# Optimization experiments

Hardware: AMD Instinct MI355X
Metric: run time of the kernel (lower is better)

Reference implementation:

```python
import jax, jax.numpy as jnp
import numpy as np

B, T, LAT = 32, 196, 256
NJ3, NJ2, NJ1 = 13, 10, 20  # joints with feature dims 3, 2, 1 (contiguous groups)
D3, D2, D1 = NJ3 * 3, NJ2 * 2, NJ1 * 1  # spans in the flat feature axis (39, 20, 20)


def setup_inputs() -> dict:
    key = jax.random.key(0)
    ks = jax.random.split(key, 13)
    s = 0.05
    return {
        "x": jax.random.normal(ks[0], (B, T, D3 + D2 + D1), dtype=jnp.float32),
        "W1_3": jax.random.normal(ks[1], (NJ3, 3, LAT), dtype=jnp.float32) * s,
        "b1_3": jax.random.normal(ks[2], (NJ3, LAT), dtype=jnp.float32) * s,
        "W2_3": jax.random.normal(ks[3], (NJ3, LAT, LAT), dtype=jnp.float32) * s,
        "b2_3": jax.random.normal(ks[4], (NJ3, LAT), dtype=jnp.float32) * s,
        "W1_2": jax.random.normal(ks[5], (NJ2, 2, LAT), dtype=jnp.float32) * s,
        "b1_2": jax.random.normal(ks[6], (NJ2, LAT), dtype=jnp.float32) * s,
        "W2_2": jax.random.normal(ks[7], (NJ2, LAT, LAT), dtype=jnp.float32) * s,
        "b2_2": jax.random.normal(ks[8], (NJ2, LAT), dtype=jnp.float32) * s,
        "W1_1": jax.random.normal(ks[9], (NJ1, 1, LAT), dtype=jnp.float32) * s,
        "b1_1": jax.random.normal(ks[10], (NJ1, LAT), dtype=jnp.float32) * s,
        "W2_1": jax.random.normal(ks[11], (NJ1, LAT, LAT), dtype=jnp.float32) * s,
        "b2_1": jax.random.normal(ks[12], (NJ1, LAT), dtype=jnp.float32) * s,
    }


def _group_mlp(xg, W1, b1, W2, b2):
    # xg: [B,T,J,d] ; W1: [J,d,LAT] ; W2: [J,LAT,LAT]
    h = jnp.einsum("btjd,jdl->btjl", xg, W1) + b1
    h = jax.nn.gelu(h)
    return jnp.einsum("btjl,jlm->btjm", h, W2) + b2


def reference(x, W1_3, b1_3, W2_3, b2_3, W1_2, b1_2, W2_2, b2_2, W1_1, b1_1, W2_1, b2_1):
    Bx, Tx, _ = x.shape
    # split the flat feature axis per joint_feature_dims and reshape into [B,T,J,d] groups
    x3 = x[..., :D3].reshape(Bx, Tx, NJ3, 3)
    x2 = x[..., D3:D3 + D2].reshape(Bx, Tx, NJ2, 2)
    x1 = x[..., D3 + D2:].reshape(Bx, Tx, NJ1, 1)
    o3 = _group_mlp(x3, W1_3, b1_3, W2_3, b2_3)
    o2 = _group_mlp(x2, W1_2, b1_2, W2_2, b2_2)
    o1 = _group_mlp(x1, W1_1, b1_1, W2_1, b2_1)
    # stack per-joint outputs in joint order -> [B,T,43,LAT]
    return jnp.concatenate([o3, o2, o1], axis=2)
```

## Files before the change

### kernel.cpp

```cpp
#include <hip/hip_runtime.h>
#include <stdint.h>

#define BT   6272
#define LAT  256
#define NJ3  13
#define NJ2  10
#define NJ1  20
#define NJ   43
#define D3   39
#define D2   20
#define XDIM 79
#define OUTROW 11008

typedef _Float16 half8  __attribute__((ext_vector_type(8)));
typedef _Float16 half4v __attribute__((ext_vector_type(4)));
typedef float    floatx4 __attribute__((ext_vector_type(4)));

__device__ __forceinline__ float fast_gelu(float h) {
    float p  = h * h;
    float u2 = h * (1.5957691216057308f + 0.0713548162f * p);
    float e  = __expf(u2);
    float r  = __builtin_amdgcn_rcpf(e + 1.0f);
    return h - h * r;
}

__global__ __launch_bounds__(256) void transpose_w2(
    const float* __restrict__ W2_3, const float* __restrict__ W2_2,
    const float* __restrict__ W2_1, _Float16* __restrict__ W2t)
{
    __shared__ float tile[64][65];
    const int bid = blockIdx.x;
    const int j   = bid >> 4;
    const int t   = bid & 15;
    const int l0  = (t >> 2) * 64;
    const int m0  = (t & 3) * 64;

    const float* W2 = (j < NJ3) ? (W2_3 + (size_t)j * 65536)
                    : (j < NJ3 + NJ2) ? (W2_2 + (size_t)(j - NJ3) * 65536)
                    : (W2_1 + (size_t)(j - NJ3 - NJ2) * 65536);

    const int tx = threadIdx.x & 15, ty = threadIdx.x >> 4;
#pragma unroll
    for (int rr = 0; rr < 4; ++rr) {
        const int row = ty + rr * 16;
        const float4 v = *(const float4*)(W2 + (size_t)(l0 + row) * 256 + m0 + tx * 4);
        tile[row][tx * 4 + 0] = v.x;
        tile[row][tx * 4 + 1] = v.y;
        tile[row][tx * 4 + 2] = v.z;
        tile[row][tx * 4 + 3] = v.w;
    }
    __syncthreads();
#pragma unroll
    for (int rr = 0; rr < 4; ++rr) {
        const int mrow = ty + rr * 16;
        const int ll   = tx * 4;
        half4v o;
        o[0] = (_Float16)tile[ll + 0][mrow];
        o[1] = (_Float16)tile[ll + 1][mrow];
        o[2] = (_Float16)tile[ll + 2][mrow];
        o[3] = (_Float16)tile[ll + 3][mrow];
        *(half4v*)(W2t + ((size_t)j * 256 + m0 + mrow) * 256 + l0 + ll) = o;
    }
}

__global__ __launch_bounds__(256, 3) void motion_main(
    const float* __restrict__ x,
    const float* __restrict__ W1_3, const float* __restrict__ b1_3, const float* __restrict__ b2_3,
    const float* __restrict__ W1_2, const float* __restrict__ b1_2, const float* __restrict__ b2_2,
    const float* __restrict__ W1_1, const float* __restrict__ b1_1, const float* __restrict__ b2_1,
    const _Float16* __restrict__ W2t,
    float* __restrict__ out)
{
    __shared__ half8 Alds[512];

    const int bid = blockIdx.x;
    const int j   = bid / 98;
    const int mt  = bid % 98;
    const int r0  = mt * 64;

    int d, xoff;
    const float *W1, *b1, *b2;
    if (j < NJ3)            { d = 3; xoff = j * 3;
                              W1 = W1_3 + j * 768;  b1 = b1_3 + j * 256;  b2 = b2_3 + j * 256; }
    else if (j < NJ3 + NJ2) { const int q = j - NJ3; d = 2; xoff = D3 + q * 2;
                              W1 = W1_2 + q * 512;  b1 = b1_2 + q * 256;  b2 = b2_2 + q * 256; }
    else                    { const int q = j - NJ3 - NJ2; d = 1; xoff = D3 + D2 + q;
                              W1 = W1_1 + q * 256;  b1 = b1_1 + q * 256;  b2 = b2_1 + q * 256; }

    const int tid  = threadIdx.x;
    const int rr   = tid >> 2;
    const int qq   = tid & 3;
    const int lane = tid & 63;
    const int wv   = tid >> 6;
    const int m16  = lane & 15;
    const int quad = lane >> 4;

    const float* xr = x + (size_t)(r0 + rr) * XDIM + xoff;
    const float xv0 = xr[0];
    const float xv1 = (d > 1) ? xr[1] : 0.0f;
    const float xv2 = (d > 2) ? xr[2] : 0.0f;

    floatx4 acc[4][4];
#pragma unroll
    for (int i = 0; i < 4; ++i)
#pragma unroll
        for (int jj = 0; jj < 4; ++jj)
            acc[i][jj] = (floatx4){0.f, 0.f, 0.f, 0.f};

    const _Float16* W2j = W2t + (size_t)j * 65536 + (size_t)(wv * 64) * 256;

    for (int kc = 0; kc < 4; ++kc) {
        __syncthreads();
#pragma unroll
        for (int run = 0; run < 2; ++run) {
            const int c  = qq * 2 + run;
            const int l0 = kc * 64 + c * 8;
            float h[8];
#pragma unroll
            for (int u = 0; u < 8; ++u) h[u] = b1[l0 + u];
#pragma unroll
            for (int u = 0; u < 8; ++u) h[u] += xv0 * W1[l0 + u];
            if (d > 1) {
#pragma unroll
                for (int u = 0; u < 8; ++u) h[u] += xv1 * W1[256 + l0 + u];
            }
            if (d > 2) {
#pragma unroll
                for (int u = 0; u < 8; ++u) h[u] += xv2 * W1[512 + l0 + u];
            }
            half8 v;
#pragma unroll
            for (int u = 0; u < 8; ++u) v[u] = (_Float16)fast_gelu(h[u]);
            const int slot = (((rr >> 4) * 2 + (c >> 2)) * 4 + (c & 3));
            Alds[slot * 16 + ((rr & 15) ^ ((slot & 3) << 1))] = v;
        }
        __syncthreads();
#pragma unroll
        for (int kk2 = 0; kk2 < 2; ++kk2) {
            half8 af[4];
#pragma unroll
            for (int i = 0; i < 4; ++i) {
                const int slot = (i * 2 + kk2) * 4 + quad;
                af[i] = Alds[slot * 16 + (m16 ^ ((slot & 3) << 1))];
            }
            const int kidx = kc * 64 + kk2 * 32 + quad * 8;
#pragma unroll
            for (int jj = 0; jj < 4; ++jj) {
                const half8 bf = *(const half8*)(W2j + (size_t)(jj * 16 + m16) * 256 + kidx);
#pragma unroll
                for (int i = 0; i < 4; ++i)
                    acc[i][jj] = __builtin_amdgcn_mfma_f32_16x16x32_f16(af[i], bf, acc[i][jj], 0, 0, 0);
            }
        }
    }

#pragma unroll
    for (int jj = 0; jj < 4; ++jj) {
        const int n   = wv * 64 + jj * 16 + m16;
        const float b2v = b2[n];
#pragma unroll
        for (int i = 0; i < 4; ++i) {
            const int rbase = r0 + i * 16 + quad * 4;
            float* op = out + (size_t)rbase * OUTROW + (size_t)j * 256 + n;
#pragma unroll
            for (int g = 0; g < 4; ++g)
                op[(size_t)g * OUTROW] = acc[i][jj][g] + b2v;
        }
    }
}

extern "C" void kernel_launch(void* const* d_in, const int* in_sizes, int n_in,
                              void* d_out, int out_size, void* d_ws, size_t ws_size,
                              hipStream_t stream) {
    const float* x    = (const float*)d_in[0];
    const float* W1_3 = (const float*)d_in[1];
    const float* b1_3 = (const float*)d_in[2];
    const float* W2_3 = (const float*)d_in[3];
    const float* b2_3 = (const float*)d_in[4];
    const float* W1_2 = (const float*)d_in[5];
    const float* b1_2 = (const float*)d_in[6];
    const float* W2_2 = (const float*)d_in[7];
    const float* b2_2 = (const float*)d_in[8];
    const float* W1_1 = (const float*)d_in[9];
    const float* b1_1 = (const float*)d_in[10];
    const float* W2_1 = (const float*)d_in[11];
    const float* b2_1 = (const float*)d_in[12];
    float* out = (float*)d_out;
    _Float16* W2t = (_Float16*)d_ws;

    transpose_w2<<<NJ * 16, 256, 0, stream>>>(W2_3, W2_2, W2_1, W2t);
    motion_main<<<NJ * 98, 256, 0, stream>>>(x, W1_3, b1_3, b2_3,
                                             W1_2, b1_2, b2_2,
                                             W1_1, b1_1, b2_1, W2t, out);
}
```

Baseline: 449.7 us.

## Double-buffer hidden activations in LDS and remap workgroups across XCDs

```diff
diff --git a/kernel.cpp b/kernel.cpp
--- a/kernel.cpp
+++ b/kernel.cpp
@@ -11,6 +11,7 @@
 #define D2   20
 #define XDIM 79
 #define OUTROW 11008
+#define NWG  (NJ * 98)
 
 typedef _Float16 half8  __attribute__((ext_vector_type(8)));
 typedef _Float16 half4v __attribute__((ext_vector_type(4)));
@@ -71,21 +72,26 @@
     const _Float16* __restrict__ W2t,
     float* __restrict__ out)
 {
-    __shared__ half8 Alds[512];
-
-    const int bid = blockIdx.x;
-    const int j   = bid / 98;
-    const int mt  = bid % 98;
+    __shared__ half8 Alds[2][512];
+
+    const int orig = blockIdx.x;
+    const int q8   = NWG >> 3, r8 = NWG & 7;
+    const int xcd  = orig & 7;
+    const int wgid = (xcd < r8 ? xcd * (q8 + 1)
+                               : r8 * (q8 + 1) + (xcd - r8) * q8) + (orig >> 3);
+
+    const int j   = wgid / 98;
+    const int mt  = wgid % 98;
     const int r0  = mt * 64;
 
     int d, xoff;
     const float *W1, *b1, *b2;
     if (j < NJ3)            { d = 3; xoff = j * 3;
                               W1 = W1_3 + j * 768;  b1 = b1_3 + j * 256;  b2 = b2_3 + j * 256; }
-    else if (j < NJ3 + NJ2) { const int q = j - NJ3; d = 2; xoff = D3 + q * 2;
-                              W1 = W1_2 + q * 512;  b1 = b1_2 + q * 256;  b2 = b2_2 + q * 256; }
-    else                    { const int q = j - NJ3 - NJ2; d = 1; xoff = D3 + D2 + q;
-                              W1 = W1_1 + q * 256;  b1 = b1_1 + q * 256;  b2 = b2_1 + q * 256; }
+    else if (j < NJ3 + NJ2) { const int qj = j - NJ3; d = 2; xoff = D3 + qj * 2;
+                              W1 = W1_2 + qj * 512;  b1 = b1_2 + qj * 256;  b2 = b2_2 + qj * 256; }
+    else                    { const int qj = j - NJ3 - NJ2; d = 1; xoff = D3 + D2 + qj;
+                              W1 = W1_1 + qj * 256;  b1 = b1_1 + qj * 256;  b2 = b2_1 + qj * 256; }
 
     const int tid  = threadIdx.x;
     const int rr   = tid >> 2;
@@ -95,10 +101,13 @@
     const int m16  = lane & 15;
     const int quad = lane >> 4;
 
-    const float* xr = x + (size_t)(r0 + rr) * XDIM + xoff;
-    const float xv0 = xr[0];
-    const float xv1 = (d > 1) ? xr[1] : 0.0f;
-    const float xv2 = (d > 2) ? xr[2] : 0.0f;
+    const float* xr  = x + (size_t)(r0 + rr) * XDIM + xoff;
+    const float  xv0 = xr[0];
+    const float  xv1 = (d > 1) ? xr[1] : 0.0f;
+    const float  xv2 = (d > 2) ? xr[2] : 0.0f;
+    const float* W1r0 = W1;
+    const float* W1r1 = W1 + ((d > 1) ? 256 : 0);
+    const float* W1r2 = W1 + ((d > 2) ? 512 : 0);
 
     floatx4 acc[4][4];
 #pragma unroll
@@ -109,8 +118,7 @@
 
     const _Float16* W2j = W2t + (size_t)j * 65536 + (size_t)(wv * 64) * 256;
 
-    for (int kc = 0; kc < 4; ++kc) {
-        __syncthreads();
+    auto compute_h = [&](int kc, int nb) {
 #pragma unroll
         for (int run = 0; run < 2; ++run) {
             const int c  = qq * 2 + run;
@@ -119,29 +127,32 @@
 #pragma unroll
             for (int u = 0; u < 8; ++u) h[u] = b1[l0 + u];
 #pragma unroll
-            for (int u = 0; u < 8; ++u) h[u] += xv0 * W1[l0 + u];
-            if (d > 1) {
-#pragma unroll
-                for (int u = 0; u < 8; ++u) h[u] += xv1 * W1[256 + l0 + u];
-            }
-            if (d > 2) {
-#pragma unroll
-                for (int u = 0; u < 8; ++u) h[u] += xv2 * W1[512 + l0 + u];
-            }
+            for (int u = 0; u < 8; ++u) h[u] += xv0 * W1r0[l0 + u];
+#pragma unroll
+            for (int u = 0; u < 8; ++u) h[u] += xv1 * W1r1[l0 + u];
+#pragma unroll
+            for (int u = 0; u < 8; ++u) h[u] += xv2 * W1r2[l0 + u];
             half8 v;
 #pragma unroll
             for (int u = 0; u < 8; ++u) v[u] = (_Float16)fast_gelu(h[u]);
             const int slot = (((rr >> 4) * 2 + (c >> 2)) * 4 + (c & 3));
-            Alds[slot * 16 + ((rr & 15) ^ ((slot & 3) << 1))] = v;
+            Alds[nb][slot * 16 + ((rr & 15) ^ ((slot & 3) << 1))] = v;
         }
-        __syncthreads();
+    };
+
+    compute_h(0, 0);
+    __syncthreads();
+
+    for (int kc = 0; kc < 4; ++kc) {
+        const int b = kc & 1;
+        if (kc < 3) compute_h(kc + 1, b ^ 1);
 #pragma unroll
         for (int kk2 = 0; kk2 < 2; ++kk2) {
             half8 af[4];
 #pragma unroll
             for (int i = 0; i < 4; ++i) {
                 const int slot = (i * 2 + kk2) * 4 + quad;
-                af[i] = Alds[slot * 16 + (m16 ^ ((slot & 3) << 1))];
+                af[i] = Alds[b][slot * 16 + (m16 ^ ((slot & 3) << 1))];
             }
             const int kidx = kc * 64 + kk2 * 32 + quad * 8;
 #pragma unroll
@@ -152,6 +163,7 @@
                     acc[i][jj] = __builtin_amdgcn_mfma_f32_16x16x32_f16(af[i], bf, acc[i][jj], 0, 0, 0);
             }
         }
+        if (kc < 3) __syncthreads();
     }
 
 #pragma unroll
@@ -189,7 +201,7 @@
     _Float16* W2t = (_Float16*)d_ws;
 
     transpose_w2<<<NJ * 16, 256, 0, stream>>>(W2_3, W2_2, W2_1, W2t);
-    motion_main<<<NJ * 98, 256, 0, stream>>>(x, W1_3, b1_3, b2_3,
-                                             W1_2, b1_2, b2_2,
-                                             W1_1, b1_1, b2_1, W2t, out);
-}
+    motion_main<<<NWG, 256, 0, stream>>>(x, W1_3, b1_3, b2_3,
+                                         W1_2, b1_2, b2_2,
+                                         W1_1, b1_1, b2_1, W2t, out);
+}
```

Result: no change. 445.2 us (-1.0%).
